# Performance work log

Hardware: AMD Instinct MI355X
Metric: run time of the kernel (lower is better)

## Reference

```python
import jax, jax.numpy as jnp
import numpy as np
import math

E = 1024
H = 16
D = E // H  # head_dim = 64
BASE = 10000.0


def rotate_half(x):
    x1, x2 = x[..., : x.shape[-1] // 2], x[..., x.shape[-1] // 2 :]
    return jnp.concatenate((-x2, x1), axis=-1)


def rope_cos_sin(seq_len, dtype):
    inv_freq = 1.0 / (BASE ** (jnp.arange(0, D, 2, dtype=jnp.float32) / D))
    t = jnp.arange(seq_len, dtype=jnp.float32)
    freqs = jnp.einsum('i,j->ij', t, inv_freq)          # [S, D/2]
    emb = jnp.concatenate((freqs, freqs), axis=-1)      # [S, D]
    return emb.astype(dtype) * 0 + jnp.cos(emb).astype(dtype), jnp.sin(emb).astype(dtype)


def setup_inputs() -> dict:
    key = jax.random.key(0)
    ks = jax.random.split(key, 12)
    B, S = 2, 2048
    s = 1.0 / math.sqrt(E)
    return {
        'query': jax.random.normal(ks[0], (B, S, E), jnp.float32),
        'key':   jax.random.normal(ks[1], (B, S, E), jnp.float32),
        'value': jax.random.normal(ks[2], (B, S, E), jnp.float32),
        'Wq': jax.random.normal(ks[3], (E, E), jnp.float32) * s,
        'bq': jnp.zeros((E,), jnp.float32),
        'Wk': jax.random.normal(ks[4], (E, E), jnp.float32) * s,
        'bk': jnp.zeros((E,), jnp.float32),
        'Wv': jax.random.normal(ks[5], (E, E), jnp.float32) * s,
        'bv': jnp.zeros((E,), jnp.float32),
        'Wo': jax.random.normal(ks[6], (E, E), jnp.float32) * s,
        'bo': jnp.zeros((E,), jnp.float32),
    }


def reference(query, key, value, Wq, bq, Wk, bk, Wv, bv, Wo, bo):
    B, S, _ = query.shape
    scale = 1.0 / math.sqrt(D)

    def heads(x, W, b):  # [B,S,E] -> [B,H,S,D]
        return (x @ W.T + b).reshape(B, S, H, D).transpose(0, 2, 1, 3)

    q = heads(query, Wq, bq)
    k = heads(key, Wk, bk)
    v = heads(value, Wv, bv)

    cos, sin = rope_cos_sin(S, q.dtype)  # [S, D] each
    cos = cos[None, None]                # [1,1,S,D]
    sin = sin[None, None]
    q = q * cos + rotate_half(q) * sin
    k = k * cos + rotate_half(k) * sin

    attn_weights = jnp.einsum('bhqd,bhkd->bhqk', q, k) * scale
    attn_weights = jax.nn.softmax(attn_weights, axis=-1)
    attn_output = jnp.einsum('bhqk,bhkd->bhqd', attn_weights, v)
    attn_output = attn_output.transpose(0, 2, 1, 3).reshape(B, S, E)
    output = attn_output @ Wo.T + bo
    return output, attn_weights
```

## Files before the change

kernel.cpp:

```cpp
#include <hip/hip_runtime.h>
#include <hip/hip_bf16.h>


#define DEV static __device__ __forceinline__

typedef __attribute__((ext_vector_type(8))) short short8;
typedef __attribute__((ext_vector_type(4))) float f32x4;
typedef unsigned short u16;

#if defined(__has_builtin)
# if __has_builtin(__builtin_amdgcn_global_load_lds)
#  define HAS_GLL 1
# endif
#endif
#ifndef HAS_GLL
# define HAS_GLL 0
#endif

DEV u16 f2bf(float x){
  unsigned u = __float_as_uint(x);
  u += 0x7fff + ((u >> 16) & 1);
  return (u16)(u >> 16);
}
DEV float bf2f(u16 h){ return __uint_as_float(((unsigned)h) << 16); }

#define MFMA(a,b,c) __builtin_amdgcn_mfma_f32_16x16x32_bf16((a),(b),(c),0,0,0)

#define LDP 72
#define TILE (128*64)
#define QSCALE 0.18033688f
#define VMCNT0   asm volatile("s_waitcnt vmcnt(0)" ::: "memory")
#define LGKM0    asm volatile("s_waitcnt lgkmcnt(0)" ::: "memory")
#define SBAR     __builtin_amdgcn_s_barrier()

DEV int SW(int row, int g){ return row*64 + (((g) ^ (row & 7)) << 3); }

DEV void stage8(const u16* __restrict__ g0, int rs, u16* tile, int r0){
  int lane = threadIdx.x & 63;
  int r = lane >> 3, gl = (lane & 7) ^ (r & 7);
  const u16* src = g0 + (size_t)r * rs + gl * 8;
#if HAS_GLL
  __builtin_amdgcn_global_load_lds((const void*)src, (void*)(tile + r0*64), 16, 0, 0);
#else
  *(short8*)&tile[(r0 + r)*64 + (lane & 7)*8] = *(const short8*)src;
#endif
}

struct PrepArgs { const float* src[7]; u16* dst[7]; int n4[7]; float* cs; };

__global__ void k_prep(PrepArgs a){
  int y = blockIdx.y;
  int t0 = blockIdx.x * blockDim.x + threadIdx.x;
  if (y == 7){
    if (t0 < 65536){
      int s = t0 >> 5, i = t0 & 31;
      float f = powf(10000.0f, -(float)i * (1.0f/32.0f));
      float ang = (float)s * f;
      a.cs[t0]         = cosf(ang);
      a.cs[65536 + t0] = sinf(ang);
    }
    return;
  }
  const float* src = a.src[y]; u16* dst = a.dst[y]; int n4 = a.n4[y];
  int st = gridDim.x * blockDim.x;
  for (int i = t0; i < n4; i += st){
    float4 v = ((const float4*)src)[i];
    ushort4 o; o.x=f2bf(v.x); o.y=f2bf(v.y); o.z=f2bf(v.z); o.w=f2bf(v.w);
    ((ushort4*)dst)[i] = o;
  }
}

__global__ __launch_bounds__(256, 2) void k_projqkv(
    const u16* __restrict__ qA, const u16* __restrict__ kA, const u16* __restrict__ vA,
    const u16* __restrict__ Wqp, const u16* __restrict__ Wkp, const u16* __restrict__ Wvp,
    const float* __restrict__ bqp, const float* __restrict__ bkp, const float* __restrict__ bvp,
    const float* __restrict__ cs,
    u16* __restrict__ qO, u16* __restrict__ kO, u16* __restrict__ vO)
{
  __shared__ __align__(16) u16 smem[4*TILE];

  const int id = blockIdx.x;
  const int wg = (id & 7) * 96 + (id >> 3);
  const int sec = wg >> 8;
  const int rem = wg & 255;
  const int n0 = (rem & 7) * 128, m0 = (rem >> 3) * 128;

  const u16* A_g = (sec==0) ? qA : (sec==1) ? kA : vA;
  const u16* W_g = (sec==0) ? Wqp : (sec==1) ? Wkp : Wvp;
  const float* bias = (sec==0) ? bqp : (sec==1) ? bkp : bvp;
  u16* out = (sec==0) ? qO : (sec==1) ? kO : vO;

  const int tid = threadIdx.x, lane = tid & 63, wv = tid >> 6;
  const int wm = wv >> 1, wn = wv & 1;
  const int l15 = lane & 15, l4 = lane >> 4;

  const f32x4 z4 = {0.f,0.f,0.f,0.f};
  f32x4 acc[4][4];
#pragma unroll
  for (int i=0;i<4;++i)
#pragma unroll
    for (int j=0;j<4;++j) acc[i][j] = z4;

  auto stageAB = [&](int kt, int buf){
    u16* Ab = smem + buf*TILE;
    u16* Bb = smem + (2+buf)*TILE;
#pragma unroll
    for (int t = 0; t < 4; ++t){
      int r0 = (wv*4 + t)*8;
      stage8(&A_g[(size_t)(m0+r0)*1024 + kt*64], 1024, Ab, r0);
      stage8(&W_g[(size_t)(n0+r0)*1024 + kt*64], 1024, Bb, r0);
    }
  };

  stageAB(0, 0);
  VMCNT0; SBAR;

  for (int kt = 0; kt < 16; ++kt){
    const int cur = kt & 1;
    if (kt < 15) stageAB(kt+1, cur^1);
    const u16* Ac = smem + cur*TILE;
    const u16* Bc = smem + (2+cur)*TILE;
#pragma unroll
    for (int ks = 0; ks < 2; ++ks){
      const int ksg = l4 + ks*4;
      short8 ah[4], bh[4];
#pragma unroll
      for (int mi=0;mi<4;++mi) ah[mi] = *(const short8*)&Ac[SW(wm*64+mi*16+l15, ksg)];
#pragma unroll
      for (int nf=0;nf<4;++nf) bh[nf] = *(const short8*)&Bc[SW(wn*64+nf*16+l15, ksg)];
#pragma unroll
      for (int mi=0;mi<4;++mi)
#pragma unroll
        for (int nf=0;nf<4;++nf)
          acc[mi][nf] = MFMA(ah[mi], bh[nf], acc[mi][nf]);
    }
    VMCNT0; SBAR;
  }

  if (sec != 2){
    const int h = (n0 + wn*64) >> 6;
    const float sc = (sec==0) ? QSCALE : 1.0f;
    float bv4[4];
#pragma unroll
    for (int nf=0;nf<4;++nf) bv4[nf] = bias[n0 + wn*64 + nf*16 + l15];
#pragma unroll
    for (int mi=0;mi<4;++mi)
#pragma unroll
      for (int r=0;r<4;++r){
        int srow = m0 + wm*64 + mi*16 + l4*4 + r;
        int b = srow >> 11, s = srow & 2047;
#pragma unroll
        for (int half=0; half<2; ++half){
          int dmod = half*16 + l15;
          float ct = cs[s*32 + dmod], st = cs[65536 + s*32 + dmod];
          float vlo = acc[mi][half  ][r] + bv4[half  ];
          float vhi = acc[mi][half+2][r] + bv4[half+2];
          float olo = (vlo*ct - vhi*st) * sc;
          float ohi = (vhi*ct + vlo*st) * sc;
          size_t base = ((size_t)(b*16 + h)*2048 + s)*64;
          out[base + dmod]      = f2bf(olo);
          out[base + dmod + 32] = f2bf(ohi);
        }
      }
  } else {
    u16* T = smem;
    const int TST = 130;
#pragma unroll
    for (int mi=0;mi<4;++mi)
#pragma unroll
      for (int nf=0;nf<4;++nf)
#pragma unroll
        for (int r=0;r<4;++r){
          int rowl = wm*64 + mi*16 + l4*4 + r;
          int coll = wn*64 + nf*16 + l15;
          T[rowl*TST + coll] = f2bf(acc[mi][nf][r] + bias[n0 + coll]);
        }
    __syncthreads();
    int col = tid >> 1, sh = tid & 1;
    int h = (n0 + col) >> 6, d = (n0 + col) & 63;
    int b = m0 >> 11;
    size_t gbase = ((size_t)(b*16 + h)*64 + d)*2048 + (m0 & 2047) + sh*64;
#pragma unroll
    for (int j=0;j<64;j+=8){
      short8 pk;
#pragma unroll
      for (int e=0;e<8;++e) pk[e] = (short)T[(sh*64 + j + e)*TST + col];
      *(short8*)&out[gbase + j] = pk;
    }
  }
}

__global__ __launch_bounds__(256, 2) void k_attn(
    const u16* __restrict__ qh, const u16* __restrict__ kh,
    const u16* __restrict__ vt,
    float* __restrict__ wout,
    u16* __restrict__ aout)
{
  __shared__ __align__(16) u16 WL[2*128*LDP];
  __shared__ float lpart[2][128];
  __shared__ float invl[128];

  const int id = blockIdx.x;
  const int xcd = id & 7, s5 = id >> 3;
  const int pair = xcd*4 + (s5 >> 4);
  const int m0 = (s5 & 15) * 128;
  const int h = pair & 15, b = pair >> 4;

  const size_t bh = (size_t)(b*16 + h);
  const u16* qh_p = qh + bh*2048*64;
  const u16* kh_p = kh + bh*2048*64;
  const u16* vt_p = vt + bh*64*2048;

  const int tid = threadIdx.x, lane = tid & 63, wv = tid >> 6;
  const int wm = wv >> 1, wn = wv & 1;
  const int l15 = lane & 15, l4 = lane >> 4;
  const f32x4 z4 = {0.f,0.f,0.f,0.f};

  auto loadK = [&](short8* KB, int jt){
    const u16* kp = kh_p + ((size_t)(jt*64 + wn*32 + l15))*64 + l4*8;
    KB[0] = *(const short8*)kp;
    KB[1] = *(const short8*)(kp + 32);
    KB[2] = *(const short8*)(kp + 1024);
    KB[3] = *(const short8*)(kp + 1024+32);
  };
  auto loadV = [&](short8* VF, int jt){
    const u16* vp = vt_p + ((size_t)(wn*32 + l15))*2048 + jt*64 + l4*8;
    VF[0] = *(const short8*)vp;
    VF[1] = *(const short8*)(vp + 32);
    VF[2] = *(const short8*)(vp + 16*2048);
    VF[3] = *(const short8*)(vp + 16*2048+32);
  };
  auto qkmma = [&](const short8* KB, f32x4 (&ZF)[4][2], const short8 (&QF)[4][2]){
#pragma unroll
    for (int mi=0;mi<4;++mi){
      ZF[mi][0] = MFMA(QF[mi][0], KB[0], ZF[mi][0]);
      ZF[mi][0] = MFMA(QF[mi][1], KB[1], ZF[mi][0]);
      ZF[mi][1] = MFMA(QF[mi][0], KB[2], ZF[mi][1]);
      ZF[mi][1] = MFMA(QF[mi][1], KB[3], ZF[mi][1]);
    }
  };

  short8 qhf[4][2];
#pragma unroll
  for (int mi=0;mi<4;++mi)
#pragma unroll
    for (int ks=0;ks<2;++ks)
      qhf[mi][ks] = *(const short8*)&qh_p[(size_t)(m0 + wm*64 + mi*16 + l15)*64 + l4*8 + ks*32];

  float lsum[4][4];
#pragma unroll
  for (int mi=0;mi<4;++mi)
#pragma unroll
    for (int r=0;r<4;++r) lsum[mi][r] = 0.f;

  auto p1body = [&](int jt, const short8* KB){
    f32x4 zf[4][2];
#pragma unroll
    for (int mi=0;mi<4;++mi){ zf[mi][0]=z4; zf[mi][1]=z4; }
    qkmma(KB, zf, qhf);
#pragma unroll
    for (int mi=0;mi<4;++mi)
#pragma unroll
      for (int r=0;r<4;++r)
        lsum[mi][r] += exp2f(zf[mi][0][r]) + exp2f(zf[mi][1][r]);
  };
  {
    short8 kbA[4], kbB[4];
    loadK(kbA, 0);
    for (int jt = 0; jt < 32; jt += 2){
      loadK(kbB, (jt+1)&31);
      p1body(jt, kbA);
      loadK(kbA, (jt+2)&31);
      p1body(jt+1, kbB);
    }
  }
#pragma unroll
  for (int mi=0;mi<4;++mi)
#pragma unroll
    for (int r=0;r<4;++r){
      float p = lsum[mi][r];
      p += __shfl_xor(p, 1, 64);
      p += __shfl_xor(p, 2, 64);
      p += __shfl_xor(p, 4, 64);
      p += __shfl_xor(p, 8, 64);
      if (l15 == 0) lpart[wn][wm*64 + mi*16 + l4*4 + r] = p;
    }
  __syncthreads();
  if (tid < 128) invl[tid] = 1.0f / (lpart[0][tid] + lpart[1][tid]);
  __syncthreads();

  float ilr[4][4];
#pragma unroll
  for (int mi=0;mi<4;++mi)
#pragma unroll
    for (int r=0;r<4;++r) ilr[mi][r] = invl[wm*64 + mi*16 + l4*4 + r];

  f32x4 oacc[4][2];
#pragma unroll
  for (int mi=0;mi<4;++mi){ oacc[mi][0]=z4; oacc[mi][1]=z4; }

  const size_t woutb = (bh*2048 + (size_t)m0)*2048;

  auto p2body = [&](int jt, const short8* KBcur, short8* KBnext, u16* WLc){
    short8 vf[4];
    loadV(vf, jt);
    loadK(KBnext, (jt+1)&31);
    f32x4 zf[4][2];
#pragma unroll
    for (int mi=0;mi<4;++mi){ zf[mi][0]=z4; zf[mi][1]=z4; }
    qkmma(KBcur, zf, qhf);
#pragma unroll
    for (int mi=0;mi<4;++mi)
#pragma unroll
      for (int r=0;r<4;++r){
        int rowl = wm*64 + mi*16 + l4*4 + r;
        float il = ilr[mi][r];
        float w0 = exp2f(zf[mi][0][r]) * il;
        float w1 = exp2f(zf[mi][1][r]) * il;
        WLc[rowl*LDP + wn*32 + l15]      = f2bf(w0);
        WLc[rowl*LDP + wn*32 + 16 + l15] = f2bf(w1);
        size_t gr = woutb + (size_t)rowl*2048 + jt*64;
        __builtin_nontemporal_store(w0, &wout[gr + wn*32 + l15]);
        __builtin_nontemporal_store(w1, &wout[gr + wn*32 + 16 + l15]);
      }
    LGKM0; SBAR;
#pragma unroll
    for (int ks=0;ks<2;++ks){
      const int ko = l4*8 + ks*32;
      short8 aw[4];
#pragma unroll
      for (int mi=0;mi<4;++mi) aw[mi] = *(const short8*)&WLc[(wm*64 + mi*16 + l15)*LDP + ko];
#pragma unroll
      for (int mi=0;mi<4;++mi){
        oacc[mi][0] = MFMA(aw[mi], vf[0 + ks], oacc[mi][0]);
        oacc[mi][1] = MFMA(aw[mi], vf[2 + ks], oacc[mi][1]);
      }
    }
  };
  {
    short8 kbA[4], kbB[4];
    loadK(kbA, 0);
    for (int jt = 0; jt < 32; jt += 2){
      p2body(jt,   kbA, kbB, WL);
      p2body(jt+1, kbB, kbA, WL + 128*LDP);
    }
  }

#pragma unroll
  for (int mi=0;mi<4;++mi)
#pragma unroll
    for (int nf=0;nf<2;++nf)
#pragma unroll
      for (int r=0;r<4;++r){
        int rowl = wm*64 + mi*16 + l4*4 + r;
        int d = wn*32 + nf*16 + l15;
        aout[((size_t)(b*2048 + m0 + rowl)*16 + h)*64 + d] = f2bf(oacc[mi][nf][r]);
      }
}

__global__ __launch_bounds__(256, 2) void k_oproj(
    const u16* __restrict__ A_g, const u16* __restrict__ W_g,
    const float* __restrict__ bias, float* __restrict__ out0)
{
  __shared__ __align__(16) u16 smem[4*TILE];
  const int id = blockIdx.x;
  const int wg = (id & 7) * 32 + (id >> 3);
  const int n0 = (wg & 7) * 128, m0 = (wg >> 3) * 128;

  const int tid = threadIdx.x, lane = tid & 63, wv = tid >> 6;
  const int wm = wv >> 1, wn = wv & 1, l15 = lane & 15, l4 = lane >> 4;
  const f32x4 z4 = {0.f,0.f,0.f,0.f};
  f32x4 acc[4][4];
#pragma unroll
  for (int i=0;i<4;++i)
#pragma unroll
    for (int j=0;j<4;++j) acc[i][j] = z4;

  auto stageAB = [&](int kt, int buf){
    u16* Ab = smem + buf*TILE;
    u16* Bb = smem + (2+buf)*TILE;
#pragma unroll
    for (int t = 0; t < 4; ++t){
      int r0 = (wv*4 + t)*8;
      stage8(&A_g[(size_t)(m0+r0)*1024 + kt*64], 1024, Ab, r0);
      stage8(&W_g[(size_t)(n0+r0)*1024 + kt*64], 1024, Bb, r0);
    }
  };

  stageAB(0, 0);
  VMCNT0; SBAR;
  for (int kt = 0; kt < 16; ++kt){
    const int cur = kt & 1;
    if (kt < 15) stageAB(kt+1, cur^1);
    const u16* Ac = smem + cur*TILE;
    const u16* Bc = smem + (2+cur)*TILE;
#pragma unroll
    for (int ks = 0; ks < 2; ++ks){
      const int ksg = l4 + ks*4;
      short8 ah[4], bhh[4];
#pragma unroll
      for (int mi=0;mi<4;++mi) ah[mi] = *(const short8*)&Ac[SW(wm*64+mi*16+l15, ksg)];
#pragma unroll
      for (int nf=0;nf<4;++nf) bhh[nf] = *(const short8*)&Bc[SW(wn*64+nf*16+l15, ksg)];
#pragma unroll
      for (int mi=0;mi<4;++mi)
#pragma unroll
        for (int nf=0;nf<4;++nf)
          acc[mi][nf] = MFMA(ah[mi], bhh[nf], acc[mi][nf]);
    }
    VMCNT0; SBAR;
  }
#pragma unroll
  for (int mi=0;mi<4;++mi)
#pragma unroll
    for (int nf=0;nf<4;++nf)
#pragma unroll
      for (int r=0;r<4;++r){
        int rowl = wm*64 + mi*16 + l4*4 + r;
        int coll = wn*64 + nf*16 + l15;
        out0[(size_t)(m0+rowl)*1024 + n0 + coll] = acc[mi][nf][r] + bias[n0+coll];
      }
}

extern "C" void kernel_launch(void* const* d_in, const int* in_sizes, int n_in,
                              void* d_out, int out_size, void* d_ws, size_t ws_size,
                              hipStream_t stream) {
  const float* query = (const float*)d_in[0];
  const float* key   = (const float*)d_in[1];
  const float* value = (const float*)d_in[2];
  const float* Wq = (const float*)d_in[3]; const float* bq = (const float*)d_in[4];
  const float* Wk = (const float*)d_in[5]; const float* bk = (const float*)d_in[6];
  const float* Wv = (const float*)d_in[7]; const float* bv = (const float*)d_in[8];
  const float* Wo = (const float*)d_in[9]; const float* bo = (const float*)d_in[10];

  float* out0 = (float*)d_out;
  float* out1 = out0 + (size_t)4096*1024;

  char* cur = (char*)d_ws;
  auto take = [&](size_t bytes)->void*{
    void* p = (void*)cur; cur += (bytes + 255) & ~(size_t)255; return p;
  };
  u16* query_hi = (u16*)take(8388608);
  u16* key_hi   = (u16*)take(8388608);
  u16* value_hi = (u16*)take(8388608);
  u16* Wq_hi = (u16*)take(2097152);
  u16* Wk_hi = (u16*)take(2097152);
  u16* Wv_hi = (u16*)take(2097152);
  u16* Wo_hi = (u16*)take(2097152);
  u16* q_hi = (u16*)take(8388608);
  u16* k_hi = (u16*)take(8388608);
  u16* vT   = (u16*)take(8388608);
  u16* attn_o = (u16*)take(8388608);
  float* cs = (float*)take(524288);

  PrepArgs pa;
  pa.src[0]=query; pa.dst[0]=query_hi; pa.n4[0]=1048576;
  pa.src[1]=key;   pa.dst[1]=key_hi;   pa.n4[1]=1048576;
  pa.src[2]=value; pa.dst[2]=value_hi; pa.n4[2]=1048576;
  pa.src[3]=Wq;    pa.dst[3]=Wq_hi;    pa.n4[3]=262144;
  pa.src[4]=Wk;    pa.dst[4]=Wk_hi;    pa.n4[4]=262144;
  pa.src[5]=Wv;    pa.dst[5]=Wv_hi;    pa.n4[5]=262144;
  pa.src[6]=Wo;    pa.dst[6]=Wo_hi;    pa.n4[6]=262144;
  pa.cs = cs;
  k_prep<<<dim3(512,8), 256, 0, stream>>>(pa);

  k_projqkv<<<768, 256, 0, stream>>>(query_hi, key_hi, value_hi,
                                     Wq_hi, Wk_hi, Wv_hi,
                                     bq, bk, bv, cs,
                                     q_hi, k_hi, vT);

  k_attn<<<512, 256, 0, stream>>>(q_hi, k_hi, vT, out1, attn_o);

  k_oproj<<<256, 256, 0, stream>>>(attn_o, Wo_hi, bo, out0);
}
```

Baseline: 237.6 us.

## Remap attention waves to split key/value columns across four waves

Changes the attention kernel's wave decomposition from a 2x2 grid (two row halves by two column halves) to four waves that each own all 128 query rows and a 16-wide slice of keys and head-dim outputs. Each wave now loads fewer K/V fragments per tile but holds all Q fragments, so K/V global loads are no longer duplicated across row-waves. This raises register pressure (8x2 Q fragments, 8 accumulators) and needs a four-way partial-sum reduction for the softmax denominator.

```diff
diff --git a/kernel.cpp b/kernel.cpp
--- a/kernel.cpp
+++ b/kernel.cpp
@@ -197,7 +197,7 @@
     u16* __restrict__ aout)
 {
   __shared__ __align__(16) u16 WL[2*128*LDP];
-  __shared__ float lpart[2][128];
+  __shared__ float lpart[4][128];
   __shared__ float invl[128];
 
   const int id = blockIdx.x;
@@ -211,71 +211,65 @@
   const u16* kh_p = kh + bh*2048*64;
   const u16* vt_p = vt + bh*64*2048;
 
-  const int tid = threadIdx.x, lane = tid & 63, wv = tid >> 6;
-  const int wm = wv >> 1, wn = wv & 1;
+  const int tid = threadIdx.x, lane = tid & 63;
+  const int wn = tid >> 6;
   const int l15 = lane & 15, l4 = lane >> 4;
   const f32x4 z4 = {0.f,0.f,0.f,0.f};
 
   auto loadK = [&](short8* KB, int jt){
-    const u16* kp = kh_p + ((size_t)(jt*64 + wn*32 + l15))*64 + l4*8;
+    const u16* kp = kh_p + ((size_t)(jt*64 + wn*16 + l15))*64 + l4*8;
     KB[0] = *(const short8*)kp;
     KB[1] = *(const short8*)(kp + 32);
-    KB[2] = *(const short8*)(kp + 1024);
-    KB[3] = *(const short8*)(kp + 1024+32);
   };
   auto loadV = [&](short8* VF, int jt){
-    const u16* vp = vt_p + ((size_t)(wn*32 + l15))*2048 + jt*64 + l4*8;
+    const u16* vp = vt_p + ((size_t)(wn*16 + l15))*2048 + jt*64 + l4*8;
     VF[0] = *(const short8*)vp;
     VF[1] = *(const short8*)(vp + 32);
-    VF[2] = *(const short8*)(vp + 16*2048);
-    VF[3] = *(const short8*)(vp + 16*2048+32);
-  };
-  auto qkmma = [&](const short8* KB, f32x4 (&ZF)[4][2], const short8 (&QF)[4][2]){
-#pragma unroll
-    for (int mi=0;mi<4;++mi){
-      ZF[mi][0] = MFMA(QF[mi][0], KB[0], ZF[mi][0]);
-      ZF[mi][0] = MFMA(QF[mi][1], KB[1], ZF[mi][0]);
-      ZF[mi][1] = MFMA(QF[mi][0], KB[2], ZF[mi][1]);
-      ZF[mi][1] = MFMA(QF[mi][1], KB[3], ZF[mi][1]);
-    }
-  };
-
-  short8 qhf[4][2];
-#pragma unroll
-  for (int mi=0;mi<4;++mi)
+  };
+  auto qkmma = [&](const short8* KB, f32x4 (&ZF)[8], const short8 (&QF)[8][2]){
+#pragma unroll
+    for (int mi=0;mi<8;++mi){
+      ZF[mi] = MFMA(QF[mi][0], KB[0], ZF[mi]);
+      ZF[mi] = MFMA(QF[mi][1], KB[1], ZF[mi]);
+    }
+  };
+
+  short8 qhf[8][2];
+#pragma unroll
+  for (int mi=0;mi<8;++mi)
 #pragma unroll
     for (int ks=0;ks<2;++ks)
-      qhf[mi][ks] = *(const short8*)&qh_p[(size_t)(m0 + wm*64 + mi*16 + l15)*64 + l4*8 + ks*32];
-
-  float lsum[4][4];
-#pragma unroll
-  for (int mi=0;mi<4;++mi)
+      qhf[mi][ks] = *(const short8*)&qh_p[(size_t)(m0 + mi*16 + l15)*64 + l4*8 + ks*32];
+
+  float lsum[8][4];
+#pragma unroll
+  for (int mi=0;mi<8;++mi)
 #pragma unroll
     for (int r=0;r<4;++r) lsum[mi][r] = 0.f;
 
-  auto p1body = [&](int jt, const short8* KB){
-    f32x4 zf[4][2];
-#pragma unroll
-    for (int mi=0;mi<4;++mi){ zf[mi][0]=z4; zf[mi][1]=z4; }
+  auto p1body = [&](const short8* KB){
+    f32x4 zf[8];
+#pragma unroll
+    for (int mi=0;mi<8;++mi) zf[mi] = z4;
     qkmma(KB, zf, qhf);
 #pragma unroll
-    for (int mi=0;mi<4;++mi)
+    for (int mi=0;mi<8;++mi)
 #pragma unroll
       for (int r=0;r<4;++r)
-        lsum[mi][r] += exp2f(zf[mi][0][r]) + exp2f(zf[mi][1][r]);
+        lsum[mi][r] += exp2f(zf[mi][r]);
   };
   {
-    short8 kbA[4], kbB[4];
+    short8 kbA[2], kbB[2];
     loadK(kbA, 0);
     for (int jt = 0; jt < 32; jt += 2){
       loadK(kbB, (jt+1)&31);
-      p1body(jt, kbA);
+      p1body(kbA);
       loadK(kbA, (jt+2)&31);
-      p1body(jt+1, kbB);
-    }
-  }
-#pragma unroll
-  for (int mi=0;mi<4;++mi)
+      p1body(kbB);
+    }
+  }
+#pragma unroll
+  for (int mi=0;mi<8;++mi)
 #pragma unroll
     for (int r=0;r<4;++r){
       float p = lsum[mi][r];
@@ -283,62 +277,56 @@
       p += __shfl_xor(p, 2, 64);
       p += __shfl_xor(p, 4, 64);
       p += __shfl_xor(p, 8, 64);
-      if (l15 == 0) lpart[wn][wm*64 + mi*16 + l4*4 + r] = p;
+      if (l15 == 0) lpart[wn][mi*16 + l4*4 + r] = p;
     }
   __syncthreads();
-  if (tid < 128) invl[tid] = 1.0f / (lpart[0][tid] + lpart[1][tid]);
+  if (tid < 128)
+    invl[tid] = 1.0f / (lpart[0][tid] + lpart[1][tid] + lpart[2][tid] + lpart[3][tid]);
   __syncthreads();
 
-  float ilr[4][4];
-#pragma unroll
-  for (int mi=0;mi<4;++mi)
-#pragma unroll
-    for (int r=0;r<4;++r) ilr[mi][r] = invl[wm*64 + mi*16 + l4*4 + r];
-
-  f32x4 oacc[4][2];
-#pragma unroll
-  for (int mi=0;mi<4;++mi){ oacc[mi][0]=z4; oacc[mi][1]=z4; }
+  float ilr[8][4];
+#pragma unroll
+  for (int mi=0;mi<8;++mi)
+#pragma unroll
+    for (int r=0;r<4;++r) ilr[mi][r] = invl[mi*16 + l4*4 + r];
+
+  f32x4 oacc[8];
+#pragma unroll
+  for (int mi=0;mi<8;++mi) oacc[mi] = z4;
 
   const size_t woutb = (bh*2048 + (size_t)m0)*2048;
 
   auto p2body = [&](int jt, const short8* KBcur, short8* KBnext, u16* WLc){
-    short8 vf[4];
+    short8 vf[2];
     loadV(vf, jt);
     loadK(KBnext, (jt+1)&31);
-    f32x4 zf[4][2];
-#pragma unroll
-    for (int mi=0;mi<4;++mi){ zf[mi][0]=z4; zf[mi][1]=z4; }
+    f32x4 zf[8];
+#pragma unroll
+    for (int mi=0;mi<8;++mi) zf[mi] = z4;
     qkmma(KBcur, zf, qhf);
 #pragma unroll
-    for (int mi=0;mi<4;++mi)
+    for (int mi=0;mi<8;++mi)
 #pragma unroll
       for (int r=0;r<4;++r){
-        int rowl = wm*64 + mi*16 + l4*4 + r;
-        float il = ilr[mi][r];
-        float w0 = exp2f(zf[mi][0][r]) * il;
-        float w1 = exp2f(zf[mi][1][r]) * il;
-        WLc[rowl*LDP + wn*32 + l15]      = f2bf(w0);
-        WLc[rowl*LDP + wn*32 + 16 + l15] = f2bf(w1);
-        size_t gr = woutb + (size_t)rowl*2048 + jt*64;
-        __builtin_nontemporal_store(w0, &wout[gr + wn*32 + l15]);
-        __builtin_nontemporal_store(w1, &wout[gr + wn*32 + 16 + l15]);
+        int rowl = mi*16 + l4*4 + r;
+        float w = exp2f(zf[mi][r]) * ilr[mi][r];
+        WLc[rowl*LDP + wn*16 + l15] = f2bf(w);
+        __builtin_nontemporal_store(w, &wout[woutb + (size_t)rowl*2048 + jt*64 + wn*16 + l15]);
       }
     LGKM0; SBAR;
 #pragma unroll
     for (int ks=0;ks<2;++ks){
       const int ko = l4*8 + ks*32;
-      short8 aw[4];
-#pragma unroll
-      for (int mi=0;mi<4;++mi) aw[mi] = *(const short8*)&WLc[(wm*64 + mi*16 + l15)*LDP + ko];
-#pragma unroll
-      for (int mi=0;mi<4;++mi){
-        oacc[mi][0] = MFMA(aw[mi], vf[0 + ks], oacc[mi][0]);
-        oacc[mi][1] = MFMA(aw[mi], vf[2 + ks], oacc[mi][1]);
-      }
+      short8 aw[8];
+#pragma unroll
+      for (int mi=0;mi<8;++mi) aw[mi] = *(const short8*)&WLc[(mi*16 + l15)*LDP + ko];
+#pragma unroll
+      for (int mi=0;mi<8;++mi)
+        oacc[mi] = MFMA(aw[mi], vf[ks], oacc[mi]);
     }
   };
   {
-    short8 kbA[4], kbB[4];
+    short8 kbA[2], kbB[2];
     loadK(kbA, 0);
     for (int jt = 0; jt < 32; jt += 2){
       p2body(jt,   kbA, kbB, WL);
@@ -347,15 +335,13 @@
   }
 
 #pragma unroll
-  for (int mi=0;mi<4;++mi)
-#pragma unroll
-    for (int nf=0;nf<2;++nf)
-#pragma unroll
-      for (int r=0;r<4;++r){
-        int rowl = wm*64 + mi*16 + l4*4 + r;
-        int d = wn*32 + nf*16 + l15;
-        aout[((size_t)(b*2048 + m0 + rowl)*16 + h)*64 + d] = f2bf(oacc[mi][nf][r]);
-      }
+  for (int mi=0;mi<8;++mi)
+#pragma unroll
+    for (int r=0;r<4;++r){
+      int rowl = mi*16 + l4*4 + r;
+      int d = wn*16 + l15;
+      aout[((size_t)(b*2048 + m0 + rowl)*16 + h)*64 + d] = f2bf(oacc[mi][r]);
+    }
 }
 
 __global__ __launch_bounds__(256, 2) void k_oproj(
```

Result: slower. 274.5 us (+15.5%).
